# Kernel tuning notes

Measured on AMD Instinct MI355X. Metric: run time of the kernel, lower is better.

Reference implementation:

```python
import jax, jax.numpy as jnp
import numpy as np

B, S, E = 4, 1024, 1280
H = 16
D = E // H  # 80


def rotate_half(x):
    x1, x2 = jnp.split(x, 2, axis=-1)
    return jnp.concatenate([-x2, x1], axis=-1)


def setup_inputs() -> dict:
    key = jax.random.key(0)
    ks = jax.random.split(key, 12)
    sc = 0.02
    x = jax.random.normal(ks[0], (B, S, E), dtype=jnp.float32)
    # variable per-item sequence lengths (each <= S), cumulative
    lens = np.array([1024, 896, 768, 640], dtype=np.int32)
    cu_seqlens = jnp.asarray(np.concatenate([[0], np.cumsum(lens)]), dtype=jnp.int32)
    # rotary cos/sin for positions 0..S-1, head_dim D
    inv_freq = 1.0 / (10000.0 ** (np.arange(0, D, 2, dtype=np.float32) / D))
    t = np.arange(S, dtype=np.float32)
    freqs = np.outer(t, inv_freq)               # [S, D/2]
    emb = np.concatenate([freqs, freqs], axis=-1)  # [S, D]
    cos = jnp.asarray(np.cos(emb), dtype=jnp.float32)
    sin = jnp.asarray(np.sin(emb), dtype=jnp.float32)
    wq = jax.random.normal(ks[1], (E, E), dtype=jnp.float32) * sc
    bq = jax.random.normal(ks[2], (E,), dtype=jnp.float32) * sc
    wk = jax.random.normal(ks[3], (E, E), dtype=jnp.float32) * sc
    bk = jax.random.normal(ks[4], (E,), dtype=jnp.float32) * sc
    wv = jax.random.normal(ks[5], (E, E), dtype=jnp.float32) * sc
    bv = jax.random.normal(ks[6], (E,), dtype=jnp.float32) * sc
    wo = jax.random.normal(ks[7], (E, E), dtype=jnp.float32) * sc
    bo = jax.random.normal(ks[8], (E,), dtype=jnp.float32) * sc
    return {"x": x, "cu_seqlens": cu_seqlens, "cos": cos, "sin": sin,
            "wq": wq, "bq": bq, "wk": wk, "bk": bk, "wv": wv, "bv": bv,
            "wo": wo, "bo": bo}


def reference(x, cu_seqlens, cos, sin, wq, bq, wk, bk, wv, bv, wo, bo):
    b, s, e = x.shape
    h, d = H, D
    # QKV projections (nn.Linear: x @ W^T + b)
    q = (x @ wq.T + bq).reshape(b, s, h, d)
    k = (x @ wk.T + bk).reshape(b, s, h, d)
    v = (x @ wv.T + bv).reshape(b, s, h, d)
    # rotary embedding (apply_rotary_pos_emb, 'normal')
    c = cos[None, :, None, :]  # [1, s, 1, d]
    sn = sin[None, :, None, :]
    q = q * c + rotate_half(q) * sn
    k = k * c + rotate_half(k) * sn
    # patch attention mask from cu_seqlens (flatten_batch=False):
    # token i attends to token j iff i < len_b and j < len_b
    seq_lens = cu_seqlens[1:] - cu_seqlens[:-1]          # [b]
    idx = jnp.arange(s)
    valid = idx[None, :] < seq_lens[:, None]             # [b, s]
    mask = valid[:, None, :, None] & valid[:, None, None, :]  # [b, 1, s, s]
    # SDPA, non-causal
    scale = 1.0 / jnp.sqrt(jnp.asarray(d, dtype=q.dtype))
    scores = jnp.einsum("bqhd,bkhd->bhqk", q, k) * scale
    scores = jnp.where(mask, scores, jnp.asarray(-1e9, dtype=scores.dtype))
    attn = jax.nn.softmax(scores, axis=-1)
    out = jnp.einsum("bhqk,bkhd->bqhd", attn, v)         # [b, s, h, d]
    out = out.reshape(b, s, e)
    # output projection
    return out @ wo.T + bo
```

## Files before the change

### kernel.cpp

```cpp
#include <hip/hip_runtime.h>
#include <hip/hip_bf16.h>

#define B_ 4
#define S_ 1024
#define E_ 1280
#define H_ 16
#define D_ 80
#define M_ (B_*S_)

typedef __hip_bfloat16 bf16;
using bf16x8 = __attribute__((ext_vector_type(8))) short;
using f32x4  = __attribute__((ext_vector_type(4))) float;

__device__ __forceinline__ float b2f(bf16 x){ return __bfloat162float(x); }
__device__ __forceinline__ bf16  f2b(float x){ return __float2bfloat16(x); }
__device__ __forceinline__ void  stf(float* p, float v){ *p = v; }
__device__ __forceinline__ void  stf(bf16*  p, float v){ *p = f2b(v); }

__device__ __forceinline__ void gload_lds16(const void* g, void* l) {
    __builtin_amdgcn_global_load_lds(
        (const __attribute__((address_space(1))) unsigned int*)g,
        (__attribute__((address_space(3))) unsigned int*)l, 16, 0, 0);
}

__global__ __launch_bounds__(256) void cvt_kernel(
    const float* __restrict__ s0, const float* __restrict__ s1,
    const float* __restrict__ s2, const float* __restrict__ s3,
    const float* __restrict__ s4,
    bf16* __restrict__ d0, bf16* __restrict__ d1, bf16* __restrict__ d2,
    bf16* __restrict__ d3, bf16* __restrict__ d4,
    int n0, int n1)
{
    const float* s; bf16* d; int n;
    switch (blockIdx.y) {
        case 0: s = s0; d = d0; n = n0; break;
        case 1: s = s1; d = d1; n = n1; break;
        case 2: s = s2; d = d2; n = n1; break;
        case 3: s = s3; d = d3; n = n1; break;
        default: s = s4; d = d4; n = n1; break;
    }
    int i = (blockIdx.x * 256 + threadIdx.x) * 8;
    if (i >= n) return;
    float4 a = *(const float4*)(s + i);
    float4 b = *(const float4*)(s + i + 4);
    bf16 t[8];
    t[0]=f2b(a.x); t[1]=f2b(a.y); t[2]=f2b(a.z); t[3]=f2b(a.w);
    t[4]=f2b(b.x); t[5]=f2b(b.y); t[6]=f2b(b.z); t[7]=f2b(b.w);
    *(uint4*)(d + i) = *(const uint4*)t;
}

template<typename TC, bool VT_OUT>
__global__ __launch_bounds__(256) void mfma_gemm_bt(
    const bf16* __restrict__ A,
    const bf16* __restrict__ W0, const bf16* __restrict__ W1, const bf16* __restrict__ W2,
    const float* __restrict__ b0, const float* __restrict__ b1, const float* __restrict__ b2,
    TC* __restrict__ C0, TC* __restrict__ C1, TC* __restrict__ C2,
    int K, int N, int ntiles)
{
    const int mat = blockIdx.y / ntiles;
    const int bn  = (blockIdx.y % ntiles) * 128;
    const int bm  = blockIdx.x * 128;
    const bf16* W; const float* bias; TC* C;
    if (mat == 0)      { W = W0; bias = b0; C = C0; }
    else if (mat == 1) { W = W1; bias = b1; C = C1; }
    else               { W = W2; bias = b2; C = C2; }

    __shared__ bf16 As[2][128][32];
    __shared__ bf16 Ws[2][128][32];

    const int tid  = threadIdx.x;
    const int lane = tid & 63;
    const int wv   = tid >> 6;
    const int wm   = (wv & 1) * 64;
    const int wn   = (wv >> 1) * 64;
    const int srow = wv * 16 + (lane >> 2);
    const int scol = (lane & 3) * 8;

    f32x4 acc[4][4] = {};

    for (int k0 = 0; k0 < K; k0 += 64) {
        __syncthreads();
        #pragma unroll
        for (int p = 0; p < 2; p++) {
            const int kc = k0 + p*32 + scol;
            gload_lds16(A + (size_t)(bm + srow)      * K + kc, &As[p][wv*16][0]);
            gload_lds16(A + (size_t)(bm + 64 + srow) * K + kc, &As[p][64 + wv*16][0]);
            gload_lds16(W + (size_t)(bn + srow)      * K + kc, &Ws[p][wv*16][0]);
            gload_lds16(W + (size_t)(bn + 64 + srow) * K + kc, &Ws[p][64 + wv*16][0]);
        }
        __syncthreads();

        const int fr = lane & 15;
        const int kq = (lane >> 4) * 8;
        #pragma unroll
        for (int p = 0; p < 2; p++) {
            bf16x8 af[4], wf[4];
            #pragma unroll
            for (int t = 0; t < 4; t++) {
                af[t] = *(const bf16x8*)&As[p][wm + t*16 + fr][kq];
                wf[t] = *(const bf16x8*)&Ws[p][wn + t*16 + fr][kq];
            }
            #pragma unroll
            for (int mt = 0; mt < 4; mt++)
                #pragma unroll
                for (int nt = 0; nt < 4; nt++)
                    acc[mt][nt] = __builtin_amdgcn_mfma_f32_16x16x32_bf16(
                        af[mt], wf[nt], acc[mt][nt], 0, 0, 0);
        }
    }

    const int col_l = lane & 15;
    const int row_l = (lane >> 4) * 4;

    if (VT_OUT && mat == 2) {
        const int btok = bm >> 10;
        const int keyb = (bm & 1023) + wm + row_l;
        #pragma unroll
        for (int nt = 0; nt < 4; nt++) {
            const int n = bn + wn + nt*16 + col_l;
            const float bv = bias[n];
            const int hh = n / 80, dd = n % 80;
            bf16* vbase = (bf16*)C + ((size_t)(btok*H_ + hh)*D_ + dd)*S_ + keyb;
            #pragma unroll
            for (int mt = 0; mt < 4; mt++) {
                union { bf16 h[4]; uint2 u; } t4;
                #pragma unroll
                for (int r = 0; r < 4; r++) t4.h[r] = f2b(acc[mt][nt][r] + bv);
                *(uint2*)&vbase[mt*16] = t4.u;
            }
        }
    } else {
        #pragma unroll
        for (int nt = 0; nt < 4; nt++) {
            const int n = bn + wn + nt*16 + col_l;
            const float bv = bias[n];
            #pragma unroll
            for (int mt = 0; mt < 4; mt++) {
                #pragma unroll
                for (int r = 0; r < 4; r++) {
                    const int m = bm + wm + mt*16 + row_l + r;
                    stf(&C[(size_t)m * N + n], acc[mt][nt][r] + bv);
                }
            }
        }
    }
}

__device__ __forceinline__ void rope8(const bf16* lo, const bf16* hi,
                                      const float* cp, const float* sp,
                                      float mul, uint4* out_lo, uint4* out_hi)
{
    union { uint4 u; bf16 h[8]; } li, hi_, lo_o, hi_o;
    li.u  = *(const uint4*)lo;
    hi_.u = *(const uint4*)hi;
    #pragma unroll
    for (int u = 0; u < 8; u++) {
        float x1 = b2f(li.h[u]), x2 = b2f(hi_.h[u]);
        float c = cp[u], s = sp[u];
        lo_o.h[u] = f2b((x1*c - x2*s) * mul);
        hi_o.h[u] = f2b((x2*c + x1*s) * mul);
    }
    *out_lo = lo_o.u;
    *out_hi = hi_o.u;
}

__global__ __launch_bounds__(256, 4) void attn_mfma(
    const bf16* __restrict__ q, const bf16* __restrict__ k, const bf16* __restrict__ vt,
    const int* __restrict__ cu, const float* __restrict__ cosp, const float* __restrict__ sinp,
    bf16* __restrict__ o)
{
    __shared__ __align__(16) char smem[38144];
    bf16* Qs  = (bf16*)smem;
    bf16* Ks  = (bf16*)(smem + 13312);
    bf16* VTs = (bf16*)(smem + 26624);

    const int L  = blockIdx.x;
    const int qt = L >> 6;
    const int g  = L & 63;
    const int b  = g >> 4;
    const int h  = g & 15;

    const int tid = threadIdx.x;
    const int lane = tid & 63, wv = tid >> 6;
    const int quad = lane >> 4, l15 = lane & 15;
    const int q0 = qt * 64;
    const int len = cu[b + 1] - cu[b];
    const float scale = 0.11180339887498949f;

    const bool uniformq = (q0 >= len);
    const bool cleanlen = ((len & 63) == 0);
    const int  ktiles   = uniformq ? 16 : (cleanlen ? (len >> 6) : 16);
    const bool domask   = !uniformq && !cleanlen;

    bf16* PT = (bf16*)(smem + wv * 2304);

    bf16x8 qf[3];
    if (!uniformq) {
        #pragma unroll
        for (int i = 0; i < 2; i++) {
            int c = tid + i * 256;
            if (c < 320) {
                int row = c / 5, pc = c % 5;
                int s = q0 + row;
                const bf16* src = q + (size_t)(b*S_ + s)*E_ + h*D_ + pc*8;
                uint4 olo, ohi;
                rope8(src, src + 40, cosp + s*D_ + pc*8, sinp + s*D_ + pc*8, scale, &olo, &ohi);
                *(uint4*)&Qs[row*104 + pc*8]      = olo;
                *(uint4*)&Qs[row*104 + (pc+5)*8]  = ohi;
            }
        }
        if (tid < 128) {
            uint4 z = make_uint4(0,0,0,0);
            int row = tid >> 1, c8 = 10 + (tid & 1);
            *(uint4*)&Qs[row*104 + c8*8] = z;
            *(uint4*)&Ks[row*104 + c8*8] = z;
        }
        __syncthreads();
        #pragma unroll
        for (int ks = 0; ks < 3; ks++)
            qf[ks] = *(const bf16x8*)&Qs[(wv*16 + l15)*104 + ks*32 + quad*8];
    } else {
        const bf16 one = f2b(1.0f);
        #pragma unroll
        for (int nt = 0; nt < 4; nt++)
            #pragma unroll
            for (int r = 0; r < 4; r++)
                PT[(quad*4 + r)*72 + nt*16 + l15] = one;
    }

    float m_r[4], l_r[4];
    #pragma unroll
    for (int r = 0; r < 4; r++) { m_r[r] = -1e30f; l_r[r] = 0.f; }
    f32x4 o_acc[5] = {};

    const bool q_full = (q0 + 64) <= len;

    for (int kt = 0; kt < ktiles; kt++) {
        __syncthreads();
        if (!uniformq) {
            #pragma unroll
            for (int i = 0; i < 2; i++) {
                int c = tid + i * 256;
                if (c < 320) {
                    int row = c / 5, pc = c % 5;
                    int s = kt*64 + row;
                    const bf16* src = k + (size_t)(b*S_ + s)*E_ + h*D_ + pc*8;
                    uint4 olo, ohi;
                    rope8(src, src + 40, cosp + s*D_ + pc*8, sinp + s*D_ + pc*8, 1.0f, &olo, &ohi);
                    *(uint4*)&Ks[row*104 + pc*8]      = olo;
                    *(uint4*)&Ks[row*104 + (pc+5)*8]  = ohi;
                }
            }
        }
        #pragma unroll
        for (int i = 0; i < 3; i++) {
            int c = tid + i * 256;
            if (c < 640) {
                int d = c >> 3, kc = c & 7;
                *(uint4*)&VTs[d*72 + kc*8] =
                    *(const uint4*)(vt + ((size_t)(b*H_ + h)*D_ + d)*S_ + kt*64 + kc*8);
            }
        }
        __syncthreads();

        if (!uniformq) {
            f32x4 s4[4];
            #pragma unroll
            for (int nt = 0; nt < 4; nt++) {
                f32x4 a0 = {};
                #pragma unroll
                for (int ks = 0; ks < 3; ks++) {
                    bf16x8 kf = *(const bf16x8*)&Ks[(nt*16 + l15)*104 + ks*32 + quad*8];
                    a0 = __builtin_amdgcn_mfma_f32_16x16x32_bf16(qf[ks], kf, a0, 0, 0, 0);
                }
                s4[nt] = a0;
            }

            float sv[4][4];
            if (!domask || (q_full && (kt*64 + 64) <= len)) {
                #pragma unroll
                for (int r = 0; r < 4; r++)
                    #pragma unroll
                    for (int nt = 0; nt < 4; nt++)
                        sv[nt][r] = s4[nt][r];
            } else {
                bool vk[4];
                #pragma unroll
                for (int nt = 0; nt < 4; nt++) vk[nt] = (kt*64 + nt*16 + l15) < len;
                #pragma unroll
                for (int r = 0; r < 4; r++) {
                    const bool vq = (q0 + wv*16 + quad*4 + r) < len;
                    #pragma unroll
                    for (int nt = 0; nt < 4; nt++)
                        sv[nt][r] = (vq && vk[nt]) ? s4[nt][r] : -1e9f;
                }
            }
            float rmax[4];
            #pragma unroll
            for (int r = 0; r < 4; r++)
                rmax[r] = fmaxf(fmaxf(sv[0][r], sv[1][r]), fmaxf(sv[2][r], sv[3][r]));
            #pragma unroll
            for (int st = 1; st < 16; st <<= 1)
                #pragma unroll
                for (int r = 0; r < 4; r++)
                    rmax[r] = fmaxf(rmax[r], __shfl_xor(rmax[r], st, 64));
            float mnew[4], alpha[4], rsum[4], p[4][4];
            #pragma unroll
            for (int r = 0; r < 4; r++) {
                mnew[r]  = fmaxf(m_r[r], rmax[r]);
                alpha[r] = __expf(m_r[r] - mnew[r]);
                float a = 0.f;
                #pragma unroll
                for (int nt = 0; nt < 4; nt++) { p[nt][r] = __expf(sv[nt][r] - mnew[r]); a += p[nt][r]; }
                rsum[r] = a;
            }
            #pragma unroll
            for (int st = 1; st < 16; st <<= 1)
                #pragma unroll
                for (int r = 0; r < 4; r++)
                    rsum[r] += __shfl_xor(rsum[r], st, 64);
            #pragma unroll
            for (int r = 0; r < 4; r++) {
                l_r[r] = l_r[r] * alpha[r] + rsum[r];
                m_r[r] = mnew[r];
            }
            #pragma unroll
            for (int dt = 0; dt < 5; dt++)
                #pragma unroll
                for (int r = 0; r < 4; r++)
                    o_acc[dt][r] *= alpha[r];
            #pragma unroll
            for (int nt = 0; nt < 4; nt++)
                #pragma unroll
                for (int r = 0; r < 4; r++)
                    PT[(quad*4 + r)*72 + nt*16 + l15] = f2b(p[nt][r]);
        }

        bf16x8 pa[2];
        #pragma unroll
        for (int ks = 0; ks < 2; ks++)
            pa[ks] = *(const bf16x8*)&PT[l15*72 + ks*32 + quad*8];
        #pragma unroll
        for (int dt = 0; dt < 5; dt++) {
            #pragma unroll
            for (int ks = 0; ks < 2; ks++) {
                bf16x8 vf = *(const bf16x8*)&VTs[(dt*16 + l15)*72 + ks*32 + quad*8];
                o_acc[dt] = __builtin_amdgcn_mfma_f32_16x16x32_bf16(pa[ks], vf, o_acc[dt], 0, 0, 0);
            }
        }
    }

    #pragma unroll
    for (int r = 0; r < 4; r++) {
        const float inv = uniformq ? (1.0f / 1024.0f) : (1.0f / l_r[r]);
        size_t row_g = (size_t)(b*S_ + q0 + wv*16 + quad*4 + r);
        #pragma unroll
        for (int dt = 0; dt < 5; dt++)
            o[row_g*E_ + h*D_ + dt*16 + l15] = f2b(o_acc[dt][r] * inv);
    }
}

extern "C" void kernel_launch(void* const* d_in, const int* in_sizes, int n_in,
                              void* d_out, int out_size, void* d_ws, size_t ws_size,
                              hipStream_t stream)
{
    const float* x    = (const float*)d_in[0];
    const int*   cu   = (const int*)  d_in[1];
    const float* cosp = (const float*)d_in[2];
    const float* sinp = (const float*)d_in[3];
    const float* wq   = (const float*)d_in[4];
    const float* bq   = (const float*)d_in[5];
    const float* wk   = (const float*)d_in[6];
    const float* bk   = (const float*)d_in[7];
    const float* wv   = (const float*)d_in[8];
    const float* bv   = (const float*)d_in[9];
    const float* wo   = (const float*)d_in[10];
    const float* bo   = (const float*)d_in[11];
    float* out = (float*)d_out;

    bf16* q   = (bf16*)d_ws;
    bf16* kk  = q   + (size_t)M_ * E_;
    bf16* vt  = kk  + (size_t)M_ * E_;
    bf16* ao  = vt  + (size_t)M_ * E_;
    bf16* xb  = ao  + (size_t)M_ * E_;
    bf16* wqb = xb  + (size_t)M_ * E_;
    bf16* wkb = wqb + (size_t)E_ * E_;
    bf16* wvb = wkb + (size_t)E_ * E_;
    bf16* wob = wvb + (size_t)E_ * E_;

    cvt_kernel<<<dim3(2560, 5), 256, 0, stream>>>(
        x, wq, wk, wv, wo, xb, wqb, wkb, wvb, wob, M_*E_, E_*E_);

    mfma_gemm_bt<bf16, true><<<dim3(M_/128, 30), 256, 0, stream>>>(
        xb, wqb, wkb, wvb, bq, bk, bv, q, kk, vt, E_, E_, 10);

    attn_mfma<<<1024, 256, 0, stream>>>(q, kk, vt, cu, cosp, sinp, ao);

    mfma_gemm_bt<float, false><<<dim3(M_/128, 10), 256, 0, stream>>>(
        ao, wob, wob, wob, bo, bo, bo, out, out, out, E_, E_, 10);
}
```

Measured before the change: 273.1 us.

## Precompute RoPE in separate kernel and read K/V directly from global in attention

Rotary embedding and the Q scaling move into a standalone elementwise kernel that rewrites q and k in place once. The attention kernel previously recomputed RoPE on every K tile for every query tile; that repeated work goes away. The attention kernel also drops its LDS staging of Q, K and V^T and the per-tile __syncthreads, loading MFMA fragments straight from global memory. The trade-offs are an extra launch plus a full read/write pass over q and k, and each wave now reads K/V from global or L2 redundantly, with strided, less coalesced accesses.

```diff
diff --git a/kernel.cpp b/kernel.cpp
--- a/kernel.cpp
+++ b/kernel.cpp
@@ -164,15 +164,32 @@
     *out_hi = hi_o.u;
 }
 
+__global__ __launch_bounds__(256) void rope_kernel(
+    bf16* __restrict__ q, bf16* __restrict__ k,
+    const float* __restrict__ cosp, const float* __restrict__ sinp)
+{
+    const int P = M_ * H_ * 5;
+    int t = blockIdx.x * 256 + threadIdx.x;
+    if (t >= 2 * P) return;
+    const bool isq = (t < P);
+    int r = isq ? t : t - P;
+    int row = r / 80;
+    int rest = r % 80;
+    int hh = rest / 5, pc = rest % 5;
+    int s = row & (S_ - 1);
+    bf16* ptr = (isq ? q : k) + (size_t)row * E_ + hh * D_ + pc * 8;
+    const float mul = isq ? 0.11180339887498949f : 1.0f;
+    uint4 olo, ohi;
+    rope8(ptr, ptr + 40, cosp + s*D_ + pc*8, sinp + s*D_ + pc*8, mul, &olo, &ohi);
+    *(uint4*)ptr        = olo;
+    *(uint4*)(ptr + 40) = ohi;
+}
+
 __global__ __launch_bounds__(256, 4) void attn_mfma(
     const bf16* __restrict__ q, const bf16* __restrict__ k, const bf16* __restrict__ vt,
-    const int* __restrict__ cu, const float* __restrict__ cosp, const float* __restrict__ sinp,
-    bf16* __restrict__ o)
-{
-    __shared__ __align__(16) char smem[38144];
-    bf16* Qs  = (bf16*)smem;
-    bf16* Ks  = (bf16*)(smem + 13312);
-    bf16* VTs = (bf16*)(smem + 26624);
+    const int* __restrict__ cu, bf16* __restrict__ o)
+{
+    __shared__ bf16 PTall[4][16][72];
 
     const int L  = blockIdx.x;
     const int qt = L >> 6;
@@ -185,40 +202,23 @@
     const int quad = lane >> 4, l15 = lane & 15;
     const int q0 = qt * 64;
     const int len = cu[b + 1] - cu[b];
-    const float scale = 0.11180339887498949f;
 
     const bool uniformq = (q0 >= len);
     const bool cleanlen = ((len & 63) == 0);
     const int  ktiles   = uniformq ? 16 : (cleanlen ? (len >> 6) : 16);
     const bool domask   = !uniformq && !cleanlen;
 
-    bf16* PT = (bf16*)(smem + wv * 2304);
+    bf16* PT = &PTall[wv][0][0];
 
     bf16x8 qf[3];
     if (!uniformq) {
-        #pragma unroll
-        for (int i = 0; i < 2; i++) {
-            int c = tid + i * 256;
-            if (c < 320) {
-                int row = c / 5, pc = c % 5;
-                int s = q0 + row;
-                const bf16* src = q + (size_t)(b*S_ + s)*E_ + h*D_ + pc*8;
-                uint4 olo, ohi;
-                rope8(src, src + 40, cosp + s*D_ + pc*8, sinp + s*D_ + pc*8, scale, &olo, &ohi);
-                *(uint4*)&Qs[row*104 + pc*8]      = olo;
-                *(uint4*)&Qs[row*104 + (pc+5)*8]  = ohi;
-            }
-        }
-        if (tid < 128) {
-            uint4 z = make_uint4(0,0,0,0);
-            int row = tid >> 1, c8 = 10 + (tid & 1);
-            *(uint4*)&Qs[row*104 + c8*8] = z;
-            *(uint4*)&Ks[row*104 + c8*8] = z;
-        }
-        __syncthreads();
-        #pragma unroll
-        for (int ks = 0; ks < 3; ks++)
-            qf[ks] = *(const bf16x8*)&Qs[(wv*16 + l15)*104 + ks*32 + quad*8];
+        const bf16* qrow = q + (size_t)(b*S_ + q0 + wv*16 + l15)*E_ + (size_t)h*D_;
+        #pragma unroll
+        for (int ks = 0; ks < 3; ks++) {
+            const int d0 = ks*32 + quad*8;
+            if (d0 < 80) qf[ks] = *(const bf16x8*)(qrow + d0);
+            else         qf[ks] = bf16x8{};
+        }
     } else {
         const bf16 one = f2b(1.0f);
         #pragma unroll
@@ -234,43 +234,21 @@
     f32x4 o_acc[5] = {};
 
     const bool q_full = (q0 + 64) <= len;
+    const bf16* vbase0 = vt + ((size_t)(b*H_ + h)*D_)*S_;
 
     for (int kt = 0; kt < ktiles; kt++) {
-        __syncthreads();
         if (!uniformq) {
-            #pragma unroll
-            for (int i = 0; i < 2; i++) {
-                int c = tid + i * 256;
-                if (c < 320) {
-                    int row = c / 5, pc = c % 5;
-                    int s = kt*64 + row;
-                    const bf16* src = k + (size_t)(b*S_ + s)*E_ + h*D_ + pc*8;
-                    uint4 olo, ohi;
-                    rope8(src, src + 40, cosp + s*D_ + pc*8, sinp + s*D_ + pc*8, 1.0f, &olo, &ohi);
-                    *(uint4*)&Ks[row*104 + pc*8]      = olo;
-                    *(uint4*)&Ks[row*104 + (pc+5)*8]  = ohi;
-                }
-            }
-        }
-        #pragma unroll
-        for (int i = 0; i < 3; i++) {
-            int c = tid + i * 256;
-            if (c < 640) {
-                int d = c >> 3, kc = c & 7;
-                *(uint4*)&VTs[d*72 + kc*8] =
-                    *(const uint4*)(vt + ((size_t)(b*H_ + h)*D_ + d)*S_ + kt*64 + kc*8);
-            }
-        }
-        __syncthreads();
-
-        if (!uniformq) {
+            const bf16* kbase = k + (size_t)(b*S_ + kt*64)*E_ + (size_t)h*D_;
             f32x4 s4[4];
             #pragma unroll
             for (int nt = 0; nt < 4; nt++) {
                 f32x4 a0 = {};
                 #pragma unroll
                 for (int ks = 0; ks < 3; ks++) {
-                    bf16x8 kf = *(const bf16x8*)&Ks[(nt*16 + l15)*104 + ks*32 + quad*8];
+                    const int d0 = ks*32 + quad*8;
+                    bf16x8 kf;
+                    if (d0 < 80) kf = *(const bf16x8*)(kbase + (size_t)(nt*16 + l15)*E_ + d0);
+                    else         kf = bf16x8{};
                     a0 = __builtin_amdgcn_mfma_f32_16x16x32_bf16(qf[ks], kf, a0, 0, 0, 0);
                 }
                 s4[nt] = a0;
@@ -340,11 +318,12 @@
         #pragma unroll
         for (int ks = 0; ks < 2; ks++)
             pa[ks] = *(const bf16x8*)&PT[l15*72 + ks*32 + quad*8];
+        const bf16* vb = vbase0 + kt*64;
         #pragma unroll
         for (int dt = 0; dt < 5; dt++) {
             #pragma unroll
             for (int ks = 0; ks < 2; ks++) {
-                bf16x8 vf = *(const bf16x8*)&VTs[(dt*16 + l15)*72 + ks*32 + quad*8];
+                bf16x8 vf = *(const bf16x8*)(vb + (size_t)(dt*16 + l15)*S_ + ks*32 + quad*8);
                 o_acc[dt] = __builtin_amdgcn_mfma_f32_16x16x32_bf16(pa[ks], vf, o_acc[dt], 0, 0, 0);
             }
         }
@@ -394,7 +373,12 @@
     mfma_gemm_bt<bf16, true><<<dim3(M_/128, 30), 256, 0, stream>>>(
         xb, wqb, wkb, wvb, bq, bk, bv, q, kk, vt, E_, E_, 10);
 
-    attn_mfma<<<1024, 256, 0, stream>>>(q, kk, vt, cu, cosp, sinp, ao);
+    {
+        int tasks = 2 * M_ * H_ * 5;
+        rope_kernel<<<(tasks + 255) / 256, 256, 0, stream>>>(q, kk, cosp, sinp);
+    }
+
+    attn_mfma<<<1024, 256, 0, stream>>>(q, kk, vt, cu, ao);
 
     mfma_gemm_bt<float, false><<<dim3(M_/128, 10), 256, 0, stream>>>(
         ao, wob, wob, wob, bo, bo, bo, out, out, out, E_, E_, 10);
```

Result: slower. 356.8 us (+30.6%).
